# Kernel tuning notes

Measured on AMD Instinct MI355X. Metric: run time of the kernel, lower is better.

Reference implementation:

```python
import jax, jax.numpy as jnp
import numpy as np

EPS = 1e-8


def setup_inputs() -> dict:
    key = jax.random.key(0)
    k1, k2, k3 = jax.random.split(key, 3)
    T, B, d, n = 1024, 8, 64, 64
    v = jax.random.normal(k1, (T, B, d), dtype=jnp.float32)
    k = jax.random.normal(k2, (T, B, n), dtype=jnp.float32)
    alpha = jax.random.uniform(k3, (T, B, n), dtype=jnp.float32)
    return {"v": v, "k": k, "alpha": alpha}


def reference(v, k, alpha):
    # v: (T,B,d), k: (T,B,n), alpha: (T,B,n) in [0,1] -> S: (T,B,d,n)
    outer = jnp.einsum('tbd,tbn->tbdn', v, k)          # (T,B,d,n)
    log_alpha = jnp.log(jnp.maximum(alpha, EPS))       # clamp_min(1e-8)
    cumprod = jnp.exp(jnp.cumsum(log_alpha, axis=0))   # (T,B,n)
    decay = cumprod / (cumprod[-1:] + EPS)             # normalize by last step
    weighted = outer * decay[:, :, None, :]            # (T,B,d,n)
    S = jnp.cumsum(weighted, axis=0)
    return S
```

## Files before the change

### kernel.cpp

```cpp
#include <hip/hip_runtime.h>

#define T_DIM 1024
#define B_DIM 8
#define D_DIM 64
#define N_DIM 64

typedef float v4f __attribute__((ext_vector_type(4)));

#define DC_CHUNKS 64
#define DC_LEN 16

#define SLAB (B_DIM * D_DIM * N_DIM)

#define WS_W 0
#define WS_PSUM (T_DIM * B_DIM * N_DIM)

__global__ __launch_bounds__(64) void decay_chunksum_kernel(
    const float* __restrict__ alpha, float* __restrict__ lsum) {
  const int b = blockIdx.x >> 6;
  const int c = blockIdx.x & 63;
  const int n = threadIdx.x;

  float s = 0.f;
#pragma unroll
  for (int i = 0; i < DC_LEN; ++i) {
    const int t = c * DC_LEN + i;
    s += logf(fmaxf(alpha[((size_t)t * B_DIM + b) * N_DIM + n], 1e-8f));
  }
  lsum[((size_t)b * DC_CHUNKS + c) * N_DIM + n] = s;
}

__global__ __launch_bounds__(64) void decay_w_kernel(
    const float* __restrict__ alpha, const float* __restrict__ kk,
    const float* __restrict__ lsum, float* __restrict__ w) {
  const int b = blockIdx.x >> 6;
  const int c = blockIdx.x & 63;
  const int n = threadIdx.x;

  const float* __restrict__ lp = lsum + (size_t)b * DC_CHUNKS * N_DIM + n;
  float pre = 0.f, tot = 0.f;
#pragma unroll 8
  for (int j = 0; j < DC_CHUNKS; ++j) {
    const float sj = lp[(size_t)j * N_DIM];
    pre += (j < c) ? sj : 0.f;
    tot += sj;
  }
  const float invden = 1.0f / (expf(tot) + 1e-8f);

  float cum = pre;
#pragma unroll
  for (int i = 0; i < DC_LEN; ++i) {
    const int t = c * DC_LEN + i;
    const size_t idx = ((size_t)t * B_DIM + b) * N_DIM + n;
    cum += logf(fmaxf(alpha[idx], 1e-8f));
    w[idx] = kk[idx] * expf(cum) * invden;
  }
}

template <int C>
__global__ __launch_bounds__(256) void chunk_psum_kernel(
    const float* __restrict__ v, float* __restrict__ ws) {
  constexpr int LEN = T_DIM / C;
  const int bid = blockIdx.x;
  const int dt = bid & 3;
  const int b  = (bid >> 2) & 7;
  const int c  = bid >> 5;
  const int tid = threadIdx.x;
  const int d  = dt * 16 + (tid >> 4);
  const int n0 = (tid & 15) * 4;

  const float* __restrict__ vp = v + (size_t)b * D_DIM + d;
  const float* __restrict__ wp = ws + WS_W + (size_t)b * N_DIM + n0;

  v4f acc = {0.f, 0.f, 0.f, 0.f};
#pragma unroll
  for (int i = 0; i < LEN; ++i) {
    const int t = c * LEN + i;
    const float vv = vp[(size_t)t * (B_DIM * D_DIM)];
    const v4f w4 = *(const v4f*)(wp + (size_t)t * (B_DIM * N_DIM));
    acc.x = fmaf(vv, w4.x, acc.x);
    acc.y = fmaf(vv, w4.y, acc.y);
    acc.z = fmaf(vv, w4.z, acc.z);
    acc.w = fmaf(vv, w4.w, acc.w);
  }
  *(v4f*)(ws + WS_PSUM + (((size_t)c * B_DIM + b) * D_DIM + d) * N_DIM + n0) = acc;
}

template <int C>
__global__ __launch_bounds__(256) void psum_prefix_kernel(float* __restrict__ ws) {
  const int q = blockIdx.x * 256 + threadIdx.x;
  v4f* __restrict__ ps  = (v4f*)(ws + WS_PSUM);
  v4f* __restrict__ pxs = ps + (size_t)C * (SLAB / 4);

  v4f run = {0.f, 0.f, 0.f, 0.f};
#pragma unroll 8
  for (int c = 0; c < C; ++c) {
    const v4f p = ps[(size_t)c * (SLAB / 4) + q];
    pxs[(size_t)c * (SLAB / 4) + q] = run;
    run.x += p.x; run.y += p.y; run.z += p.z; run.w += p.w;
  }
}

template <int C>
__global__ __launch_bounds__(256) void scan_store_kernel(
    const float* __restrict__ v, const float* __restrict__ ws,
    float* __restrict__ out) {
  constexpr int LEN = T_DIM / C;
  const int bid = blockIdx.x;
  const int dt = bid & 3;
  const int b  = (bid >> 2) & 7;
  const int c  = bid >> 5;
  const int tid = threadIdx.x;
  const int d  = dt * 16 + (tid >> 4);
  const int n0 = (tid & 15) * 4;

  const float* __restrict__ vp = v + (size_t)b * D_DIM + d;
  const float* __restrict__ wp = ws + WS_W + (size_t)b * N_DIM + n0;
  const float* __restrict__ px = ws + WS_PSUM + (size_t)C * SLAB +
                                 (((size_t)c * B_DIM + b) * D_DIM + d) * N_DIM + n0;

  v4f acc = *(const v4f*)px;

#pragma unroll
  for (int i = 0; i < LEN; ++i) {
    const int t = c * LEN + i;
    const float vv = vp[(size_t)t * (B_DIM * D_DIM)];
    const v4f w4 = *(const v4f*)(wp + (size_t)t * (B_DIM * N_DIM));
    acc.x = fmaf(vv, w4.x, acc.x);
    acc.y = fmaf(vv, w4.y, acc.y);
    acc.z = fmaf(vv, w4.z, acc.z);
    acc.w = fmaf(vv, w4.w, acc.w);
    *(v4f*)(out + (((size_t)t * B_DIM + b) * D_DIM + d) * N_DIM + n0) = acc;
  }
}

template <int C>
static void launch_all(const float* v, const float* k, const float* alpha,
                       float* out, float* ws, hipStream_t stream) {
  float* lsum = ws + WS_PSUM + (size_t)2 * C * SLAB;
  decay_chunksum_kernel<<<B_DIM * DC_CHUNKS, 64, 0, stream>>>(alpha, lsum);
  decay_w_kernel<<<B_DIM * DC_CHUNKS, 64, 0, stream>>>(alpha, k, lsum, ws + WS_W);
  chunk_psum_kernel<C><<<C * B_DIM * 4, 256, 0, stream>>>(v, ws);
  psum_prefix_kernel<C><<<SLAB / 4 / 256, 256, 0, stream>>>(ws);
  scan_store_kernel<C><<<C * B_DIM * 4, 256, 0, stream>>>(v, ws, out);
}

extern "C" void kernel_launch(void* const* d_in, const int* in_sizes, int n_in,
                              void* d_out, int out_size, void* d_ws, size_t ws_size,
                              hipStream_t stream) {
  const float* v     = (const float*)d_in[0];
  const float* k     = (const float*)d_in[1];
  const float* alpha = (const float*)d_in[2];
  float* out = (float*)d_out;
  float* ws  = (float*)d_ws;

  const size_t need64 =
      (size_t)(WS_PSUM + 2 * 64 * SLAB + B_DIM * DC_CHUNKS * N_DIM) * sizeof(float);
  if (ws_size >= need64) {
    launch_all<64>(v, k, alpha, out, ws, stream);
  } else {
    launch_all<16>(v, k, alpha, out, ws, stream);
  }
}
```

Measured before the change: 164.8 us.

## Fuse chunk partial sums, prefix and scan into one redundant-recompute kernel

New measurement: 261.6 us. 58.7% more time.

```diff
diff --git a/kernel.cpp b/kernel.cpp
--- a/kernel.cpp
+++ b/kernel.cpp
@@ -10,10 +10,8 @@
 #define DC_CHUNKS 64
 #define DC_LEN 16
 
-#define SLAB (B_DIM * D_DIM * N_DIM)
-
 #define WS_W 0
-#define WS_PSUM (T_DIM * B_DIM * N_DIM)
+#define WS_LSUM (T_DIM * B_DIM * N_DIM)
 
 __global__ __launch_bounds__(64) void decay_chunksum_kernel(
     const float* __restrict__ alpha, float* __restrict__ lsum) {
@@ -58,8 +56,9 @@
 }
 
 template <int C>
-__global__ __launch_bounds__(256) void chunk_psum_kernel(
-    const float* __restrict__ v, float* __restrict__ ws) {
+__global__ __launch_bounds__(256) void scan_fused_kernel(
+    const float* __restrict__ v, const float* __restrict__ ws,
+    float* __restrict__ out) {
   constexpr int LEN = T_DIM / C;
   const int bid = blockIdx.x;
   const int dt = bid & 3;
@@ -73,55 +72,21 @@
   const float* __restrict__ wp = ws + WS_W + (size_t)b * N_DIM + n0;
 
   v4f acc = {0.f, 0.f, 0.f, 0.f};
-#pragma unroll
-  for (int i = 0; i < LEN; ++i) {
-    const int t = c * LEN + i;
-    const float vv = vp[(size_t)t * (B_DIM * D_DIM)];
-    const v4f w4 = *(const v4f*)(wp + (size_t)t * (B_DIM * N_DIM));
-    acc.x = fmaf(vv, w4.x, acc.x);
-    acc.y = fmaf(vv, w4.y, acc.y);
-    acc.z = fmaf(vv, w4.z, acc.z);
-    acc.w = fmaf(vv, w4.w, acc.w);
+
+  for (int j = 0; j < c; ++j) {
+#pragma unroll 8
+    for (int i = 0; i < LEN; ++i) {
+      const int t = j * LEN + i;
+      const float vv = vp[(size_t)t * (B_DIM * D_DIM)];
+      const v4f w4 = *(const v4f*)(wp + (size_t)t * (B_DIM * N_DIM));
+      acc.x = fmaf(vv, w4.x, acc.x);
+      acc.y = fmaf(vv, w4.y, acc.y);
+      acc.z = fmaf(vv, w4.z, acc.z);
+      acc.w = fmaf(vv, w4.w, acc.w);
+    }
   }
-  *(v4f*)(ws + WS_PSUM + (((size_t)c * B_DIM + b) * D_DIM + d) * N_DIM + n0) = acc;
-}
 
-template <int C>
-__global__ __launch_bounds__(256) void psum_prefix_kernel(float* __restrict__ ws) {
-  const int q = blockIdx.x * 256 + threadIdx.x;
-  v4f* __restrict__ ps  = (v4f*)(ws + WS_PSUM);
-  v4f* __restrict__ pxs = ps + (size_t)C * (SLAB / 4);
-
-  v4f run = {0.f, 0.f, 0.f, 0.f};
 #pragma unroll 8
-  for (int c = 0; c < C; ++c) {
-    const v4f p = ps[(size_t)c * (SLAB / 4) + q];
-    pxs[(size_t)c * (SLAB / 4) + q] = run;
-    run.x += p.x; run.y += p.y; run.z += p.z; run.w += p.w;
-  }
-}
-
-template <int C>
-__global__ __launch_bounds__(256) void scan_store_kernel(
-    const float* __restrict__ v, const float* __restrict__ ws,
-    float* __restrict__ out) {
-  constexpr int LEN = T_DIM / C;
-  const int bid = blockIdx.x;
-  const int dt = bid & 3;
-  const int b  = (bid >> 2) & 7;
-  const int c  = bid >> 5;
-  const int tid = threadIdx.x;
-  const int d  = dt * 16 + (tid >> 4);
-  const int n0 = (tid & 15) * 4;
-
-  const float* __restrict__ vp = v + (size_t)b * D_DIM + d;
-  const float* __restrict__ wp = ws + WS_W + (size_t)b * N_DIM + n0;
-  const float* __restrict__ px = ws + WS_PSUM + (size_t)C * SLAB +
-                                 (((size_t)c * B_DIM + b) * D_DIM + d) * N_DIM + n0;
-
-  v4f acc = *(const v4f*)px;
-
-#pragma unroll
   for (int i = 0; i < LEN; ++i) {
     const int t = c * LEN + i;
     const float vv = vp[(size_t)t * (B_DIM * D_DIM)];
@@ -134,17 +99,6 @@
   }
 }
 
-template <int C>
-static void launch_all(const float* v, const float* k, const float* alpha,
-                       float* out, float* ws, hipStream_t stream) {
-  float* lsum = ws + WS_PSUM + (size_t)2 * C * SLAB;
-  decay_chunksum_kernel<<<B_DIM * DC_CHUNKS, 64, 0, stream>>>(alpha, lsum);
-  decay_w_kernel<<<B_DIM * DC_CHUNKS, 64, 0, stream>>>(alpha, k, lsum, ws + WS_W);
-  chunk_psum_kernel<C><<<C * B_DIM * 4, 256, 0, stream>>>(v, ws);
-  psum_prefix_kernel<C><<<SLAB / 4 / 256, 256, 0, stream>>>(ws);
-  scan_store_kernel<C><<<C * B_DIM * 4, 256, 0, stream>>>(v, ws, out);
-}
-
 extern "C" void kernel_launch(void* const* d_in, const int* in_sizes, int n_in,
                               void* d_out, int out_size, void* d_ws, size_t ws_size,
                               hipStream_t stream) {
@@ -154,11 +108,8 @@
   float* out = (float*)d_out;
   float* ws  = (float*)d_ws;
 
-  const size_t need64 =
-      (size_t)(WS_PSUM + 2 * 64 * SLAB + B_DIM * DC_CHUNKS * N_DIM) * sizeof(float);
-  if (ws_size >= need64) {
-    launch_all<64>(v, k, alpha, out, ws, stream);
-  } else {
-    launch_all<16>(v, k, alpha, out, ws, stream);
-  }
+  float* lsum = ws + WS_LSUM;
+  decay_chunksum_kernel<<<B_DIM * DC_CHUNKS, 64, 0, stream>>>(alpha, lsum);
+  decay_w_kernel<<<B_DIM * DC_CHUNKS, 64, 0, stream>>>(alpha, k, lsum, ws + WS_W);
+  scan_fused_kernel<32><<<32 * B_DIM * 4, 256, 0, stream>>>(v, ws, out);
 }
```
